# Performance work log

Hardware: AMD Instinct MI355X
Metric: run time of the kernel (lower is better)

Reference implementation:

```python
import jax, jax.numpy as jnp
import numpy as np

TOKEN_SELF_ATTN_VALUE = -50000.0


def setup_inputs() -> dict:
    key = jax.random.key(0)
    k1, k2, k3 = jax.random.split(key, 3)
    batch, seqlen, dim = 16, 4096, 64
    n_hashes, bucket_size = 8, 64
    n_buckets = seqlen // bucket_size  # 64
    qk = jax.random.normal(k1, (batch, seqlen, dim), dtype=jnp.float32)
    v = jax.random.normal(k2, (batch, seqlen, dim), dtype=jnp.float32)
    # random rotations for LSH hashing: (dim, n_hashes, n_buckets // 2)
    rotations = jax.random.normal(k3, (dim, n_hashes, n_buckets // 2), dtype=jnp.float32)
    return {"qk": qk, "v": v, "rotations": rotations}


def reference(qk, v, rotations):
    batch, seqlen, dim = qk.shape
    n_hashes = rotations.shape[1]
    n_buckets = 2 * rotations.shape[2]
    bucket_size = seqlen // n_buckets

    # ---- hash_vectors (rehash_each_round=True, no hash dropout) ----
    rotated = jnp.einsum('btf,fhi->bhti', qk, rotations)       # (b, h, t, nb/2)
    rotated = jnp.concatenate([rotated, -rotated], axis=-1)    # (b, h, t, nb)
    buckets = jnp.argmax(rotated, axis=-1)                     # (b, h, t)
    offsets = (jnp.arange(n_hashes) * n_buckets)[None, :, None]
    buckets = (buckets + offsets).reshape(batch, n_hashes * seqlen)

    # ---- sort tokens by (bucket, position) ----
    ticker = jnp.arange(n_hashes * seqlen)
    buckets_and_t = seqlen * buckets + (ticker % seqlen)[None, :]
    sticker = jnp.argsort(buckets_and_t, axis=-1)              # keys are unique
    undo_sort = jnp.argsort(sticker, axis=-1)
    st = sticker % seqlen                                      # original positions

    sqk = jnp.take_along_axis(qk, st[:, :, None], axis=1)      # (b, h*t, d)
    sv = jnp.take_along_axis(v, st[:, :, None], axis=1)

    chunk_size = n_hashes * n_buckets
    bq_t = st.reshape(batch, chunk_size, bucket_size)
    bqk = sqk.reshape(batch, chunk_size, bucket_size, dim)
    bv = sv.reshape(batch, chunk_size, bucket_size, dim)

    bq = bqk
    # F.normalize(p=2, eps=1e-12)
    bk = bqk / jnp.maximum(jnp.linalg.norm(bqk, axis=-1, keepdims=True), 1e-12)

    def look_one_back(x):
        return jnp.concatenate([x, jnp.roll(x, 1, axis=1)], axis=2)

    bk = look_one_back(bk)
    bv = look_one_back(bv)
    bkv_t = look_one_back(bq_t)

    dots = jnp.einsum('bcie,bcje->bcij', bq, bk) * (dim ** -0.5)  # (b, chunks, i, 2i)

    # self-attention mask (causal=False, no input masks by default)
    self_mask = bq_t[:, :, :, None] == bkv_t[:, :, None, :]
    dots = jnp.where(self_mask, TOKEN_SELF_ATTN_VALUE, dots)

    dots_logsumexp = jax.scipy.special.logsumexp(dots, axis=-1, keepdims=True)
    probs = jnp.exp(dots - dots_logsumexp)
    bo = jnp.einsum('bcij,bcje->bcie', probs, bv)

    so = bo.reshape(batch, -1, dim)                   # (b, h*t, d)
    slogits = dots_logsumexp.reshape(batch, -1)       # (b, h*t)

    # unsort back to original token order
    o = jnp.take_along_axis(so, undo_sort[:, :, None], axis=1)
    logits = jnp.take_along_axis(slogits, undo_sort, axis=1)

    o = o.reshape(batch, n_hashes, seqlen, dim)
    logits = logits.reshape(batch, n_hashes, seqlen, 1)

    # combine hash rounds weighted by their logsumexps
    w = jnp.exp(logits - jax.scipy.special.logsumexp(logits, axis=1, keepdims=True))
    out = jnp.sum(o * w, axis=1)                      # (b, t, d)
    return out
```

## Files before the change

### kernel.cpp

```cpp
#include <hip/hip_runtime.h>
#include <hip/hip_fp16.h>
#include <hip/hip_bf16.h>

#define BATCH  16
#define SEQ    4096
#define DIM    64
#define NHASH  8
#define NCHUNK 512
#define SB     72

typedef __attribute__((ext_vector_type(8))) short short8;
typedef __attribute__((ext_vector_type(4))) float floatx4;

__device__ __forceinline__ void hi16_store_cvt(const float* xs, short* dst) {
    union { __hip_bfloat162 h2[8]; uint4 u4[2]; } U;
#pragma unroll
    for (int u = 0; u < 8; ++u)
        U.h2[u] = __float22bfloat162_rn(make_float2(xs[2*u], xs[2*u + 1]));
    *(uint4*)(dst)     = U.u4[0];
    *(uint4*)(dst + 8) = U.u4[1];
}
__device__ __forceinline__ unsigned pk_bf16(float a, float b) {
    union { __hip_bfloat162 h2; unsigned u; } U;
    U.h2 = __float22bfloat162_rn(make_float2(a, b));
    return U.u;
}

__device__ __forceinline__ void argmax_store(
    const float* a, int gid, int h, int* __restrict__ buckets)
{
    float best = a[0]; int bi = 0;
#pragma unroll
    for (int i = 1; i < 32; ++i) { if (a[i] > best) { best = a[i]; bi = i; } }
#pragma unroll
    for (int i = 0; i < 32; ++i) { float nv = -a[i]; if (nv > best) { best = nv; bi = i + 32; } }
    int b = gid >> 12, t = gid & 4095;
    buckets[((size_t)b * NHASH + h) * SEQ + t] = bi;
}

__global__ __launch_bounds__(256, 4) void lsh_hash_kernel(
    const float* __restrict__ qk, const float* __restrict__ rot,
    int* __restrict__ buckets)
{
    __shared__ float rs[64 * 64];
    int tid = threadIdx.x;
    int tb   = blockIdx.x >> 2;
    int hsel = blockIdx.x & 3;

    {
        const float4* rg = (const float4*)rot;
#pragma unroll
        for (int j = 0; j < 4; ++j) {
            int idx4 = j * 256 + tid;
            int f = idx4 >> 4, r4 = idx4 & 15;
            ((float4*)rs)[idx4] = rg[f * 64 + hsel * 16 + r4];
        }
    }
    __syncthreads();

    int tt = tid & 127;
    int hh = tid >> 7;
    int gid0 = tb * 256 + tt;
    int gid1 = gid0 + 128;
    const float* q0 = qk + (size_t)gid0 * DIM;
    const float* q1 = qk + (size_t)gid1 * DIM;
    const float* rbase = rs + hh * 32;

    float a0[32], a1[32];
#pragma unroll
    for (int i = 0; i < 32; ++i) { a0[i] = 0.f; a1[i] = 0.f; }

#pragma unroll 1
    for (int ft = 0; ft < 8; ++ft) {
        float qa[8], qb[8];
        *(float4*)&qa[0] = *(const float4*)(q0 + ft * 8);
        *(float4*)&qa[4] = *(const float4*)(q0 + ft * 8 + 4);
        *(float4*)&qb[0] = *(const float4*)(q1 + ft * 8);
        *(float4*)&qb[4] = *(const float4*)(q1 + ft * 8 + 4);
#pragma unroll
        for (int f8 = 0; f8 < 8; ++f8) {
            const float* rp = rbase + (ft * 8 + f8) * 64;
            float x0 = qa[f8], x1 = qb[f8];
#pragma unroll
            for (int i = 0; i < 32; ++i) {
                float r = rp[i];
                a0[i] = fmaf(x0, r, a0[i]);
                a1[i] = fmaf(x1, r, a1[i]);
            }
        }
    }

    int h = hsel * 2 + hh;
    argmax_store(a0, gid0, h, buckets);
    argmax_store(a1, gid1, h, buckets);
}

__global__ __launch_bounds__(256) void lsh_sort_kernel(
    const int* __restrict__ buckets, int* __restrict__ st)
{
    __shared__ int hist[256 * 65];
    __shared__ int seg[256];
    __shared__ int base[64];

    int bh = blockIdx.x;
    int tid = threadIdx.x;
    int w = tid >> 6, lane = tid & 63;

    for (int i = tid; i < 256 * 65; i += 256) hist[i] = 0;

    int myb[16];
    {
        const int4* bp4 = (const int4*)(buckets + (size_t)bh * SEQ);
#pragma unroll
        for (int u4 = 0; u4 < 4; ++u4) {
            int4 bb = bp4[tid * 4 + u4];
            myb[u4*4+0] = bb.x; myb[u4*4+1] = bb.y;
            myb[u4*4+2] = bb.z; myb[u4*4+3] = bb.w;
        }
    }
    __syncthreads();
    int* hrow = &hist[tid * 65];
#pragma unroll
    for (int u = 0; u < 16; ++u) hrow[myb[u]] += 1;
    __syncthreads();

    {
        int run = 0;
        for (int tp = 0; tp < 64; ++tp) {
            int idx = (w * 64 + tp) * 65 + lane;
            int c0 = hist[idx];
            hist[idx] = run;
            run += c0;
        }
        seg[w * 64 + lane] = run;
    }
    __syncthreads();
    if (tid < 64) {
        int s0 = seg[lane], s1 = seg[64 + lane], s2 = seg[128 + lane], s3 = seg[192 + lane];
        seg[lane] = 0; seg[64 + lane] = s0;
        seg[128 + lane] = s0 + s1; seg[192 + lane] = s0 + s1 + s2;
        int tot = s0 + s1 + s2 + s3;
        int x = tot;
#pragma unroll
        for (int d = 1; d < 64; d <<= 1) {
            int y = __shfl_up(x, d, 64);
            if (lane >= d) x += y;
        }
        base[lane] = x - tot;
    }
    __syncthreads();

    int* op = st + (size_t)bh * SEQ;
#pragma unroll
    for (int u = 0; u < 16; ++u) {
        int bb = myb[u];
        int local = hrow[bb];
        hrow[bb] = local + 1;
        int pos = base[bb] + seg[w * 64 + bb] + local;
        op[pos] = tid * 16 + u;
    }
}

__global__ __launch_bounds__(256, 6) void lsh_attn_kernel(
    const float* __restrict__ qk, const float* __restrict__ v,
    const int* __restrict__ st, __half* __restrict__ Obuf, float* __restrict__ Dbuf)
{
    __shared__ short Khi[64 * SB];
    __shared__ short Vhi[64 * SB];
    __shared__ int   tk[64];
    __shared__ float lds_pad[2048];

    int tid  = threadIdx.x;
    {
        volatile float* vp = lds_pad;
        vp[tid] = 0.f;
    }
    int lane = tid & 63;
    int w    = tid >> 6;
    int quad = lane >> 4;
    int l15  = lane & 15;

    int B  = blockIdx.x;
    int bc = ((B & 7) << 10) | (B >> 3);
    int b = bc >> 9, c = bc & (NCHUNK - 1);
    int cm = (c + NCHUNK - 1) & (NCHUNK - 1);

    const int*   stb = st + (size_t)b * (NHASH * SEQ);
    const float* qkb = qk + (size_t)b * SEQ * DIM;
    const float* vb  = v  + (size_t)b * SEQ * DIM;

    short8 qH[2];
    int qt;
    {
        qt = stb[c * 64 + 16 * w + l15];
        const float* qp = qkb + (size_t)qt * DIM + 8 * quad;
#pragma unroll
        for (int kb = 0; kb < 2; ++kb) {
            float xs[8];
            *(float4*)&xs[0] = *(const float4*)(qp + 32 * kb);
            *(float4*)&xs[4] = *(const float4*)(qp + 32 * kb + 4);
            union { __hip_bfloat162 h2[4]; short8 s; } Uq;
#pragma unroll
            for (int u = 0; u < 4; ++u)
                Uq.h2[u] = __float22bfloat162_rn(make_float2(xs[2*u], xs[2*u + 1]));
            qH[kb] = Uq.s;
        }
    }
    int tqr[4];
#pragma unroll
    for (int r = 0; r < 4; ++r) tqr[r] = stb[c * 64 + 16 * w + quad * 4 + r];

    float   Dacc = 0.f;
    floatx4 oacc[4];
#pragma unroll
    for (int a = 0; a < 4; ++a) oacc[a] = (floatx4){0.f, 0.f, 0.f, 0.f};

    int sA = l15 + ((lane & 16) ? 32 : 0);
    int sB = sA + 16;
    bool qhi = (lane >= 32);

    for (int half = 0; half < 2; ++half) {
        int ck = half ? cm : c;
        __syncthreads();

        {
            int r = tid >> 2, s = tid & 3;
            int trow = stb[ck * 64 + r];
            if (s == 0) tk[r] = trow;
            const float4* k4 = (const float4*)(qkb + (size_t)trow * DIM + s * 16);
            float xs[16];
            *(float4*)&xs[0]  = k4[0];
            *(float4*)&xs[4]  = k4[1];
            *(float4*)&xs[8]  = k4[2];
            *(float4*)&xs[12] = k4[3];
            float ss = 0.f;
#pragma unroll
            for (int u = 0; u < 16; ++u) ss += xs[u] * xs[u];
            ss += __shfl_xor(ss, 1);
            ss += __shfl_xor(ss, 2);
            float sc = 1.0f / fmaxf(sqrtf(ss), 1e-12f);
#pragma unroll
            for (int u = 0; u < 16; ++u) xs[u] *= sc;
            hi16_store_cvt(xs, &Khi[r * SB + s * 16]);
        }
        {
            float xs[16];
#pragma unroll
            for (int u = 0; u < 16; ++u) {
                int trow = stb[ck * 64 + w * 16 + u];
                xs[u] = vb[(size_t)trow * DIM + lane];
            }
            hi16_store_cvt(xs, &Vhi[lane * SB + w * 16]);
        }
        __syncthreads();

        floatx4 dt[4];
#pragma unroll
        for (int jt = 0; jt < 4; ++jt) dt[jt] = (floatx4){0.f, 0.f, 0.f, 0.f};
#pragma unroll
        for (int kb = 0; kb < 2; ++kb) {
#pragma unroll
            for (int jt = 0; jt < 4; ++jt) {
                short8 kf = *(const short8*)&Khi[(16 * jt + l15) * SB + kb * 32 + quad * 8];
                dt[jt] = __builtin_amdgcn_mfma_f32_16x16x32_bf16(kf, qH[kb], dt[jt], 0, 0, 0);
            }
        }

        unsigned U[8];
#pragma unroll
        for (int jt = 0; jt < 4; ++jt) {
            int4 tkq = *(const int4*)&tk[16 * jt + quad * 4];
            float p0 = (qt == tkq.x) ? 0.f : __expf(dt[jt][0] * 0.125f);
            float p1 = (qt == tkq.y) ? 0.f : __expf(dt[jt][1] * 0.125f);
            float p2 = (qt == tkq.z) ? 0.f : __expf(dt[jt][2] * 0.125f);
            float p3 = (qt == tkq.w) ? 0.f : __expf(dt[jt][3] * 0.125f);
            Dacc += (p0 + p1) + (p2 + p3);
            U[2*jt]     = pk_bf16(p0, p1);
            U[2*jt + 1] = pk_bf16(p2, p3);
        }

#pragma unroll
        for (int kb = 0; kb < 2; ++kb) {
            unsigned xA0 = (unsigned)__shfl((int)U[4*kb + 0], sA, 64);
            unsigned yA0 = (unsigned)__shfl((int)U[4*kb + 2], sA, 64);
            unsigned xA1 = (unsigned)__shfl((int)U[4*kb + 1], sA, 64);
            unsigned yA1 = (unsigned)__shfl((int)U[4*kb + 3], sA, 64);
            unsigned xB0 = (unsigned)__shfl((int)U[4*kb + 0], sB, 64);
            unsigned yB0 = (unsigned)__shfl((int)U[4*kb + 2], sB, 64);
            unsigned xB1 = (unsigned)__shfl((int)U[4*kb + 1], sB, 64);
            unsigned yB1 = (unsigned)__shfl((int)U[4*kb + 3], sB, 64);
            union { uint4 u; short8 s; } A;
            A.u.x = qhi ? yA0 : xA0;
            A.u.y = qhi ? yA1 : xA1;
            A.u.z = qhi ? yB0 : xB0;
            A.u.w = qhi ? yB1 : xB1;
#pragma unroll
            for (int a = 0; a < 4; ++a) {
                short8 bH = *(const short8*)&Vhi[(16 * a + l15) * SB + kb * 32 + quad * 8];
                oacc[a] = __builtin_amdgcn_mfma_f32_16x16x32_bf16(A.s, bH, oacc[a], 0, 0, 0);
            }
        }
    }

    int h = c >> 6;
#pragma unroll
    for (int r = 0; r < 4; ++r) {
        int t = tqr[r];
        size_t rowb = ((size_t)(b * SEQ + t) * NHASH + h) * DIM;
#pragma unroll
        for (int a = 0; a < 4; ++a)
            Obuf[rowb + 16 * a + l15] = __float2half(oacc[a][r]);
    }
    Dacc += __shfl_xor(Dacc, 16);
    Dacc += __shfl_xor(Dacc, 32);
    if (lane < 16) Dbuf[(size_t)(b * SEQ + qt) * NHASH + h] = Dacc;
}

__global__ __launch_bounds__(256) void lsh_combine_tok(
    const __half* __restrict__ Obuf, const float* __restrict__ Dbuf,
    float* __restrict__ out)
{
    int gid = blockIdx.x * 256 + threadIdx.x;
    int d4 = gid & 15;
    int bt = gid >> 4;

    const __half* op = Obuf + (size_t)bt * (NHASH * DIM) + d4 * 4;
    const float*  dp = Dbuf + (size_t)bt * NHASH;

    float4 n = make_float4(0.f, 0.f, 0.f, 0.f);
    float den = 0.f;
#pragma unroll
    for (int h = 0; h < NHASH; ++h) {
        uint2 u = *(const uint2*)(op + h * DIM);
        __half2 p01 = *(__half2*)&u.x;
        __half2 p23 = *(__half2*)&u.y;
        float2 f01 = __half22float2(p01);
        float2 f23 = __half22float2(p23);
        den += dp[h];
        n.x += f01.x; n.y += f01.y; n.z += f23.x; n.w += f23.y;
    }
    float invd = 1.0f / den;
    float4 r; r.x = n.x*invd; r.y = n.y*invd; r.z = n.z*invd; r.w = n.w*invd;
    ((float4*)out)[gid] = r;
}

extern "C" void kernel_launch(void* const* d_in, const int* in_sizes, int n_in,
                              void* d_out, int out_size, void* d_ws, size_t ws_size,
                              hipStream_t stream)
{
    const float* qk  = (const float*)d_in[0];
    const float* v   = (const float*)d_in[1];
    const float* rot = (const float*)d_in[2];
    float* out = (float*)d_out;

    char* w = (char*)d_ws;
    int*    buckets = (int*)(w);
    int*    st      = (int*)(w + 2097152);
    __half* Obuf    = (__half*)(w + 4194304);
    float*  Dbuf    = (float*)(w + 4194304 + 67108864);

    lsh_hash_kernel<<<1024, 256, 0, stream>>>(qk, rot, buckets);
    lsh_sort_kernel<<<128, 256, 0, stream>>>(buckets, st);
    lsh_attn_kernel<<<8192, 256, 0, stream>>>(qk, v, st, Obuf, Dbuf);
    lsh_combine_tok<<<4096, 256, 0, stream>>>(Obuf, Dbuf, out);
}
```

Before: 192.8 us.

## Retile LSH hash kernel so each thread computes 8 tokens by 8 rotations

The hash kernel's per-thread work changes from 2 tokens × 32 rotation columns to 8 tokens × 8 columns. Rotation values are now held in registers and reused across tokens, and the bucket argmax is reduced across four lanes with xor shuffles and a tie-break on the lower index. The aim is to cut LDS reads per FMA and improve reuse. In exchange the strided global loads of qk are less coalesced, and launch bounds drop from 4 to 3 blocks per SM to give each thread more registers.

Result: slower. 234.2 us (+21.4%).

```diff
diff --git a/kernel.cpp b/kernel.cpp
--- a/kernel.cpp
+++ b/kernel.cpp
@@ -26,19 +26,7 @@
     return U.u;
 }
 
-__device__ __forceinline__ void argmax_store(
-    const float* a, int gid, int h, int* __restrict__ buckets)
-{
-    float best = a[0]; int bi = 0;
-#pragma unroll
-    for (int i = 1; i < 32; ++i) { if (a[i] > best) { best = a[i]; bi = i; } }
-#pragma unroll
-    for (int i = 0; i < 32; ++i) { float nv = -a[i]; if (nv > best) { best = nv; bi = i + 32; } }
-    int b = gid >> 12, t = gid & 4095;
-    buckets[((size_t)b * NHASH + h) * SEQ + t] = bi;
-}
-
-__global__ __launch_bounds__(256, 4) void lsh_hash_kernel(
+__global__ __launch_bounds__(256, 3) void lsh_hash_kernel(
     const float* __restrict__ qk, const float* __restrict__ rot,
     int* __restrict__ buckets)
 {
@@ -58,41 +46,71 @@
     }
     __syncthreads();
 
-    int tt = tid & 127;
-    int hh = tid >> 7;
-    int gid0 = tb * 256 + tt;
-    int gid1 = gid0 + 128;
-    const float* q0 = qk + (size_t)gid0 * DIM;
-    const float* q1 = qk + (size_t)gid1 * DIM;
-    const float* rbase = rs + hh * 32;
-
-    float a0[32], a1[32];
-#pragma unroll
-    for (int i = 0; i < 32; ++i) { a0[i] = 0.f; a1[i] = 0.f; }
+    int hh   = tid >> 7;
+    int th   = (tid >> 6) & 1;
+    int lane = tid & 63;
+    int l15  = lane & 15;
+    int quad = lane >> 4;
+    int h = hsel * 2 + hh;
+
+    int tok0 = tb * 256 + th * 128 + l15;
+    const float* qb = qk + (size_t)tok0 * DIM;
+    const float* rbase = rs + hh * 32 + quad * 8;
+
+    float acc[8][8];
+#pragma unroll
+    for (int t = 0; t < 8; ++t)
+#pragma unroll
+        for (int i = 0; i < 8; ++i) acc[t][i] = 0.f;
 
 #pragma unroll 1
     for (int ft = 0; ft < 8; ++ft) {
-        float qa[8], qb[8];
-        *(float4*)&qa[0] = *(const float4*)(q0 + ft * 8);
-        *(float4*)&qa[4] = *(const float4*)(q0 + ft * 8 + 4);
-        *(float4*)&qb[0] = *(const float4*)(q1 + ft * 8);
-        *(float4*)&qb[4] = *(const float4*)(q1 + ft * 8 + 4);
+        float rt[8][8];
 #pragma unroll
         for (int f8 = 0; f8 < 8; ++f8) {
-            const float* rp = rbase + (ft * 8 + f8) * 64;
-            float x0 = qa[f8], x1 = qb[f8];
-#pragma unroll
-            for (int i = 0; i < 32; ++i) {
-                float r = rp[i];
-                a0[i] = fmaf(x0, r, a0[i]);
-                a1[i] = fmaf(x1, r, a1[i]);
+            *(float4*)&rt[f8][0] = *(const float4*)(rbase + (ft * 8 + f8) * 64);
+            *(float4*)&rt[f8][4] = *(const float4*)(rbase + (ft * 8 + f8) * 64 + 4);
+        }
+#pragma unroll
+        for (int t = 0; t < 8; ++t) {
+            float qv[8];
+            *(float4*)&qv[0] = *(const float4*)(qb + (size_t)(16 * t) * DIM + ft * 8);
+            *(float4*)&qv[4] = *(const float4*)(qb + (size_t)(16 * t) * DIM + ft * 8 + 4);
+#pragma unroll
+            for (int f8 = 0; f8 < 8; ++f8) {
+                float x = qv[f8];
+#pragma unroll
+                for (int i = 0; i < 8; ++i)
+                    acc[t][i] = fmaf(x, rt[f8][i], acc[t][i]);
             }
         }
     }
 
-    int h = hsel * 2 + hh;
-    argmax_store(a0, gid0, h, buckets);
-    argmax_store(a1, gid1, h, buckets);
+#pragma unroll
+    for (int t = 0; t < 8; ++t) {
+        float bv = acc[t][0]; int bi = quad * 8;
+#pragma unroll
+        for (int i = 1; i < 8; ++i) {
+            float v = acc[t][i];
+            if (v > bv) { bv = v; bi = quad * 8 + i; }
+        }
+#pragma unroll
+        for (int i = 0; i < 8; ++i) {
+            float v = -acc[t][i];
+            if (v > bv) { bv = v; bi = 32 + quad * 8 + i; }
+        }
+#pragma unroll
+        for (int d = 16; d < 64; d <<= 1) {
+            float ov = __shfl_xor(bv, d, 64);
+            int   oi = __shfl_xor(bi, d, 64);
+            if (ov > bv || (ov == bv && oi < bi)) { bv = ov; bi = oi; }
+        }
+        if (quad == 0) {
+            int g = tok0 + 16 * t;
+            int b = g >> 12, tt = g & 4095;
+            buckets[((size_t)b * NHASH + h) * SEQ + tt] = bi;
+        }
+    }
 }
 
 __global__ __launch_bounds__(256) void lsh_sort_kernel(
```
